# Optimization experiments

Measured on AMD Instinct MI355X. Metric: run time of the kernel, lower is better.

## Reference

```python
import jax, jax.numpy as jnp
import numpy as np

KQ = 512
NEG = -1e9


def setup_inputs() -> dict:
    key = jax.random.key(0)
    k1, k2, k3, k4, k5 = jax.random.split(key, 5)
    B, NQ, NK, D, V, O = 16, 1024, 2048, 512, 512, 256
    return {
        "keys": jax.random.normal(k1, (B, NK, D), dtype=jnp.float32),
        "queries": jax.random.normal(k2, (B, NQ, D), dtype=jnp.float32),
        "values": jax.random.normal(k3, (B, NK, V), dtype=jnp.float32),
        "mask": jax.random.randint(k4, (B, NQ, NK), 0, 2, dtype=jnp.int32),
        "W_resize": jax.random.normal(k5, (O, V), dtype=jnp.float32) * (1.0 / np.sqrt(V)),
        "b_resize": jnp.zeros((O,), dtype=jnp.float32),
    }


def reference(keys, queries, values, mask, W_resize, b_resize):
    # score: scaled dot product  [B, NQ, NK]
    logits = jnp.einsum("bqd,bkd->bqk", queries, keys) / jnp.sqrt(jnp.float32(KQ))
    logits = jnp.where(mask == 0, jnp.float32(NEG), logits)
    attn = jax.nn.softmax(logits, axis=-1)
    # context: [B, NQ, V]
    context = jnp.einsum("bqk,bkv->bqv", attn, values)
    # resize to out_size
    context = jnp.einsum("bqv,ov->bqo", context, W_resize) + b_resize
    return context
```

## Files before the change

### kernel.cpp

```cpp
#include <hip/hip_runtime.h>

#define BB   16
#define NQ   1024
#define NK   2048
#define DD   512
#define VV   512
#define OO   256
#define SCALE 0.044194173824159216f

typedef __attribute__((ext_vector_type(4))) float f32x4;
typedef __attribute__((ext_vector_type(8))) short s16x8;

#define AS1(p) ((const __attribute__((address_space(1))) void*)(p))
#define AS3(p) ((__attribute__((address_space(3))) void*)(p))

__device__ __forceinline__ unsigned short f2bf(float f) {
  unsigned u = __float_as_uint(f);
  u += 0x7fffu + ((u >> 16) & 1u);
  return (unsigned short)(u >> 16);
}
__device__ __forceinline__ float bf2f(unsigned short b) {
  return __uint_as_float(((unsigned)b) << 16);
}

__device__ __forceinline__ void gemm_bt_core(
    const unsigned short* __restrict__ Abase,
    const unsigned short* __restrict__ Bbase,
    int K,
    unsigned short* As, unsigned short* Bs,
    f32x4 acc[4][4])
{
  const int t = threadIdx.x;
  const int w = t >> 6;
  const int l = t & 63;
  const int srow = l >> 2;
  const int scol = (l & 3) * 8;
  const int r0 = (w * 2 + 0) * 16 + srow;
  const int r1 = (w * 2 + 1) * 16 + srow;
  const int lds0 = (w * 2 + 0) * 512 + l * 8;
  const int lds1 = (w * 2 + 1) * 512 + l * 8;
  const int wm = (w >> 1) * 64;
  const int wn = (w & 1) * 64;
  const int lm = l & 15;
  const int lq = l >> 4;

  for (int kt = 0; kt < K; kt += 32) {
    __builtin_amdgcn_global_load_lds(AS1(Abase + (size_t)r0 * K + kt + scol), AS3(As + lds0), 16, 0, 0);
    __builtin_amdgcn_global_load_lds(AS1(Abase + (size_t)r1 * K + kt + scol), AS3(As + lds1), 16, 0, 0);
    __builtin_amdgcn_global_load_lds(AS1(Bbase + (size_t)r0 * K + kt + scol), AS3(Bs + lds0), 16, 0, 0);
    __builtin_amdgcn_global_load_lds(AS1(Bbase + (size_t)r1 * K + kt + scol), AS3(Bs + lds1), 16, 0, 0);
    __syncthreads();
    s16x8 af[4], bfr[4];
    #pragma unroll
    for (int i = 0; i < 4; ++i) {
      af[i]  = *(const s16x8*)(As + (wm + i * 16 + lm) * 32 + lq * 8);
      bfr[i] = *(const s16x8*)(Bs + (wn + i * 16 + lm) * 32 + lq * 8);
    }
    #pragma unroll
    for (int mi = 0; mi < 4; ++mi)
      #pragma unroll
      for (int ni = 0; ni < 4; ++ni)
        acc[mi][ni] = __builtin_amdgcn_mfma_f32_16x16x32_bf16(af[mi], bfr[ni], acc[mi][ni], 0, 0, 0);
    __syncthreads();
  }
}


#define CS_STRIDE 136

__global__ __launch_bounds__(256)
void qk_kernel(const unsigned short* __restrict__ Qb,
               const unsigned short* __restrict__ Kb,
               const int* __restrict__ mask,
               unsigned short* __restrict__ S,
               float* __restrict__ sums)
{
  const int b  = blockIdx.z;
  const int tm = blockIdx.y;
  const int tn = blockIdx.x;
  __shared__ unsigned short smem[128 * CS_STRIDE];
  unsigned short* As = smem;
  unsigned short* Bs = smem + 4096;
  unsigned short* Cs = smem;
  f32x4 acc[4][4];
  #pragma unroll
  for (int i = 0; i < 4; ++i)
    #pragma unroll
    for (int j = 0; j < 4; ++j) acc[i][j] = (f32x4){0.f, 0.f, 0.f, 0.f};

  gemm_bt_core(Qb + ((size_t)b * NQ + tm * 128) * DD,
               Kb + ((size_t)b * NK + tn * 128) * DD, DD, As, Bs, acc);

  const int t = threadIdx.x, w = t >> 6, l = t & 63;
  const int wm = (w >> 1) * 64, wn = (w & 1) * 64;
  const int lm = l & 15, lq = l >> 4;
  #pragma unroll
  for (int mi = 0; mi < 4; ++mi)
    #pragma unroll
    for (int ni = 0; ni < 4; ++ni)
      #pragma unroll
      for (int r = 0; r < 4; ++r)
        Cs[(wm + mi * 16 + lq * 4 + r) * CS_STRIDE + wn + ni * 16 + lm] =
            f2bf(acc[mi][ni][r] * SCALE);
  __syncthreads();

  const int trow = t >> 4, tcol = (t & 15) * 8;
  #pragma unroll
  for (int it = 0; it < 8; ++it) {
    const int row = it * 16 + trow;
    const int gq = tm * 128 + row;
    const size_t gbase = ((size_t)b * NQ + gq) * NK + tn * 128 + tcol;
    s16x8 v = *(const s16x8*)(Cs + row * CS_STRIDE + tcol);
    const int4 m0 = *(const int4*)(mask + gbase);
    const int4 m1 = *(const int4*)(mask + gbase + 4);
    float e[8];
    e[0] = m0.x ? __expf(bf2f((unsigned short)v[0])) : 0.f;
    e[1] = m0.y ? __expf(bf2f((unsigned short)v[1])) : 0.f;
    e[2] = m0.z ? __expf(bf2f((unsigned short)v[2])) : 0.f;
    e[3] = m0.w ? __expf(bf2f((unsigned short)v[3])) : 0.f;
    e[4] = m1.x ? __expf(bf2f((unsigned short)v[4])) : 0.f;
    e[5] = m1.y ? __expf(bf2f((unsigned short)v[5])) : 0.f;
    e[6] = m1.z ? __expf(bf2f((unsigned short)v[6])) : 0.f;
    e[7] = m1.w ? __expf(bf2f((unsigned short)v[7])) : 0.f;
    float sp = 0.f;
    #pragma unroll
    for (int j = 0; j < 8; ++j) sp += e[j];
    #pragma unroll
    for (int off = 8; off > 0; off >>= 1) sp += __shfl_down(sp, off, 16);
    if ((t & 15) == 0) atomicAdd(&sums[(size_t)b * NQ + gq], sp);
    s16x8 o;
    #pragma unroll
    for (int j = 0; j < 8; ++j) o[j] = (short)f2bf(e[j]);
    *(s16x8*)(S + gbase) = o;
  }
}

__global__ __launch_bounds__(256)
void pv_kernel(const unsigned short* __restrict__ P,
               const unsigned short* __restrict__ Vt,
               const float* __restrict__ sums,
               unsigned short* __restrict__ Ctx)
{
  const int b  = blockIdx.z;
  const int tm = blockIdx.y;
  const int tn = blockIdx.x;
  __shared__ unsigned short smem[128 * CS_STRIDE];
  __shared__ float Ls[128];
  unsigned short* As = smem;
  unsigned short* Bs = smem + 4096;
  unsigned short* Cs = smem;
  const int t = threadIdx.x;
  if (t < 128) Ls[t] = 1.0f / sums[(size_t)b * NQ + tm * 128 + t];
  f32x4 acc[4][4];
  #pragma unroll
  for (int i = 0; i < 4; ++i)
    #pragma unroll
    for (int j = 0; j < 4; ++j) acc[i][j] = (f32x4){0.f, 0.f, 0.f, 0.f};

  gemm_bt_core(P  + ((size_t)b * NQ + tm * 128) * NK,
               Vt + ((size_t)b * VV + tn * 128) * NK, NK, As, Bs, acc);

  const int w = t >> 6, l = t & 63;
  const int wm = (w >> 1) * 64, wn = (w & 1) * 64;
  const int lm = l & 15, lq = l >> 4;
  #pragma unroll
  for (int mi = 0; mi < 4; ++mi)
    #pragma unroll
    for (int ni = 0; ni < 4; ++ni)
      #pragma unroll
      for (int r = 0; r < 4; ++r) {
        const int row = wm + mi * 16 + lq * 4 + r;
        Cs[row * CS_STRIDE + wn + ni * 16 + lm] = f2bf(acc[mi][ni][r] * Ls[row]);
      }
  __syncthreads();
  const int trow = t >> 4, tcol = (t & 15) * 8;
  #pragma unroll
  for (int it = 0; it < 8; ++it) {
    const int row = it * 16 + trow;
    s16x8 v = *(const s16x8*)(Cs + row * CS_STRIDE + tcol);
    *(s16x8*)(Ctx + ((size_t)b * NQ + tm * 128 + row) * VV + tn * 128 + tcol) = v;
  }
}

#define CSF_STRIDE 136
__global__ __launch_bounds__(256)
void rs_kernel(const unsigned short* __restrict__ Ctx,
               const unsigned short* __restrict__ Wb,
               const float* __restrict__ bias,
               float* __restrict__ out)
{
  const int tm = blockIdx.y;
  const int tn = blockIdx.x;
  __shared__ float smemf[128 * CSF_STRIDE];
  unsigned short* As = (unsigned short*)smemf;
  unsigned short* Bs = (unsigned short*)smemf + 4096;
  float* Cs = smemf;
  f32x4 acc[4][4];
  #pragma unroll
  for (int i = 0; i < 4; ++i)
    #pragma unroll
    for (int j = 0; j < 4; ++j) acc[i][j] = (f32x4){0.f, 0.f, 0.f, 0.f};

  gemm_bt_core(Ctx + (size_t)tm * 128 * VV,
               Wb + (size_t)tn * 128 * VV, VV, As, Bs, acc);

  const int t = threadIdx.x, w = t >> 6, l = t & 63;
  const int wm = (w >> 1) * 64, wn = (w & 1) * 64;
  const int lm = l & 15, lq = l >> 4;
  #pragma unroll
  for (int mi = 0; mi < 4; ++mi)
    #pragma unroll
    for (int ni = 0; ni < 4; ++ni)
      #pragma unroll
      for (int r = 0; r < 4; ++r)
        Cs[(wm + mi * 16 + lq * 4 + r) * CSF_STRIDE + wn + ni * 16 + lm] = acc[mi][ni][r];
  __syncthreads();
  const int trow = t >> 4, tcol = (t & 15) * 8;
  #pragma unroll
  for (int it = 0; it < 8; ++it) {
    const int row = it * 16 + trow;
    f32x4 a = *(const f32x4*)(Cs + row * CSF_STRIDE + tcol);
    f32x4 c = *(const f32x4*)(Cs + row * CSF_STRIDE + tcol + 4);
    const int gn = tn * 128 + tcol;
    const f32x4 b0 = *(const f32x4*)(bias + gn);
    const f32x4 b1 = *(const f32x4*)(bias + gn + 4);
    a += b0; c += b1;
    float* o = out + (size_t)(tm * 128 + row) * OO + gn;
    *(f32x4*)o = a;
    *(f32x4*)(o + 4) = c;
  }
}

__global__ __launch_bounds__(256)
void cvt_kernel(const float* __restrict__ in, unsigned short* __restrict__ out, int n8)
{
  const int i = blockIdx.x * 256 + threadIdx.x;
  if (i >= n8) return;
  const float4* p = (const float4*)in + (size_t)i * 2;
  const float4 a = p[0], b = p[1];
  s16x8 o;
  o[0] = (short)f2bf(a.x); o[1] = (short)f2bf(a.y);
  o[2] = (short)f2bf(a.z); o[3] = (short)f2bf(a.w);
  o[4] = (short)f2bf(b.x); o[5] = (short)f2bf(b.y);
  o[6] = (short)f2bf(b.z); o[7] = (short)f2bf(b.w);
  ((s16x8*)out)[i] = o;
}

#define VT_STRIDE 68
__global__ __launch_bounds__(256)
void vt_kernel(const float* __restrict__ V, unsigned short* __restrict__ Vt)
{
  const int b  = blockIdx.z;
  const int k0 = blockIdx.y * 64;
  const int v0 = blockIdx.x * 64;
  __shared__ float tile[64 * VT_STRIDE];
  const int t = threadIdx.x;
  const int lr = t >> 4, lc4 = (t & 15) * 4;
  #pragma unroll
  for (int j = 0; j < 4; ++j) {
    const int row = lr + j * 16;
    const float4 x = *(const float4*)(V + ((size_t)b * NK + k0 + row) * VV + v0 + lc4);
    *(float4*)(tile + row * VT_STRIDE + lc4) = x;
  }
  __syncthreads();
  const int vr = t >> 3, kx = (t & 7) * 8;
  #pragma unroll
  for (int j = 0; j < 2; ++j) {
    const int v = vr + j * 32;
    s16x8 o;
    #pragma unroll
    for (int i = 0; i < 8; ++i) o[i] = (short)f2bf(tile[(kx + i) * VT_STRIDE + v]);
    *(s16x8*)(Vt + ((size_t)b * VV + v0 + v) * NK + k0 + kx) = o;
  }
}

__global__ __launch_bounds__(256)
void zero_kernel(float* __restrict__ p, int n)
{
  const int i = blockIdx.x * 256 + threadIdx.x;
  if (i < n) p[i] = 0.f;
}

extern "C" void kernel_launch(void* const* d_in, const int* in_sizes, int n_in,
                              void* d_out, int out_size, void* d_ws, size_t ws_size,
                              hipStream_t stream)
{
  const float* keys    = (const float*)d_in[0];
  const float* queries = (const float*)d_in[1];
  const float* values  = (const float*)d_in[2];
  const int*   mask    = (const int*)  d_in[3];
  const float* W       = (const float*)d_in[4];
  const float* bias    = (const float*)d_in[5];
  float* out = (float*)d_out;

  char* ws = (char*)d_ws;
  unsigned short* Qb = (unsigned short*)(ws);
  unsigned short* Kb = (unsigned short*)(ws + (16ull << 20));
  unsigned short* Vt = (unsigned short*)(ws + (48ull << 20));
  unsigned short* Wb = (unsigned short*)(ws + (80ull << 20));
  unsigned short* S  = (unsigned short*)(ws + (81ull << 20));
  float* sums        = (float*)(ws + (145ull << 20));
  unsigned short* Ctx = Qb;

  cvt_kernel<<<dim3(4096), 256, 0, stream>>>(queries, Qb, (BB * NQ * DD) / 8);
  cvt_kernel<<<dim3(8192), 256, 0, stream>>>(keys, Kb, (BB * NK * DD) / 8);
  cvt_kernel<<<dim3(64),   256, 0, stream>>>(W, Wb, (OO * VV) / 8);
  vt_kernel<<<dim3(VV / 64, NK / 64, BB), 256, 0, stream>>>(values, Vt);
  zero_kernel<<<dim3(64), 256, 0, stream>>>(sums, BB * NQ);

  qk_kernel<<<dim3(NK / 128, NQ / 128, BB), 256, 0, stream>>>(Qb, Kb, mask, S, sums);
  pv_kernel<<<dim3(VV / 128, NQ / 128, BB), 256, 0, stream>>>(S, Vt, sums, Ctx);
  rs_kernel<<<dim3(OO / 128, (BB * NQ) / 128, 1), 256, 0, stream>>>(Ctx, Wb, bias, out);
}
```

Measured before the change: 460.9 us.

## Reassociate attention output projection as P·(V·Wᵀ) and merge kernel launches

Precomputes V·Wᵀ per batch (NK×256), so the attention-probability GEMM contracts against a 256-wide matrix instead of 512 and the separate resize GEMM disappears. The VW GEMM runs inside the same launch as the QK/softmax blocks, and all conversions plus the zeroing of sums are merged into one prep kernel. The V transpose is dropped because VWt is written already transposed. The cost is an extra bf16 rounding of V·W before the P product, a different accumulation order, and smaller 64-row tiles in the final GEMM.

```diff
diff --git a/kernel.cpp b/kernel.cpp
--- a/kernel.cpp
+++ b/kernel.cpp
@@ -22,6 +22,8 @@
 __device__ __forceinline__ float bf2f(unsigned short b) {
   return __uint_as_float(((unsigned)b) << 16);
 }
+
+#define MFMA16(a, b, c) __builtin_amdgcn_mfma_f32_16x16x32_bf16(a, b, c, 0, 0, 0)
 
 __device__ __forceinline__ void gemm_bt_core(
     const unsigned short* __restrict__ Abase,
@@ -60,7 +62,7 @@
     for (int mi = 0; mi < 4; ++mi)
       #pragma unroll
       for (int ni = 0; ni < 4; ++ni)
-        acc[mi][ni] = __builtin_amdgcn_mfma_f32_16x16x32_bf16(af[mi], bfr[ni], acc[mi][ni], 0, 0, 0);
+        acc[mi][ni] = MFMA16(af[mi], bfr[ni], acc[mi][ni]);
     __syncthreads();
   }
 }
@@ -69,173 +71,190 @@
 #define CS_STRIDE 136
 
 __global__ __launch_bounds__(256)
-void qk_kernel(const unsigned short* __restrict__ Qb,
-               const unsigned short* __restrict__ Kb,
-               const int* __restrict__ mask,
-               unsigned short* __restrict__ S,
-               float* __restrict__ sums)
-{
-  const int b  = blockIdx.z;
-  const int tm = blockIdx.y;
-  const int tn = blockIdx.x;
+void qkvw_kernel(const unsigned short* __restrict__ Qb,
+                 const unsigned short* __restrict__ Kb,
+                 const unsigned short* __restrict__ Vb,
+                 const unsigned short* __restrict__ Wb,
+                 const int* __restrict__ mask,
+                 unsigned short* __restrict__ P,
+                 unsigned short* __restrict__ VWt,
+                 float* __restrict__ sums)
+{
   __shared__ unsigned short smem[128 * CS_STRIDE];
   unsigned short* As = smem;
   unsigned short* Bs = smem + 4096;
   unsigned short* Cs = smem;
+  const int bid = blockIdx.x;
+  const int t = threadIdx.x, w = t >> 6, l = t & 63;
+  const int wm = (w >> 1) * 64, wn = (w & 1) * 64;
+  const int lm = l & 15, lq = l >> 4;
+  const int trow = t >> 4, tcol = (t & 15) * 8;
+
   f32x4 acc[4][4];
   #pragma unroll
   for (int i = 0; i < 4; ++i)
     #pragma unroll
     for (int j = 0; j < 4; ++j) acc[i][j] = (f32x4){0.f, 0.f, 0.f, 0.f};
 
-  gemm_bt_core(Qb + ((size_t)b * NQ + tm * 128) * DD,
-               Kb + ((size_t)b * NK + tn * 128) * DD, DD, As, Bs, acc);
+  if (bid < 2048) {
+    const int b  = bid >> 7;
+    const int tm = (bid >> 4) & 7;
+    const int tn = bid & 15;
+
+    gemm_bt_core(Qb + ((size_t)b * NQ + tm * 128) * DD,
+                 Kb + ((size_t)b * NK + tn * 128) * DD, DD, As, Bs, acc);
+
+    #pragma unroll
+    for (int mi = 0; mi < 4; ++mi)
+      #pragma unroll
+      for (int ni = 0; ni < 4; ++ni)
+        #pragma unroll
+        for (int r = 0; r < 4; ++r)
+          Cs[(wm + mi * 16 + lq * 4 + r) * CS_STRIDE + wn + ni * 16 + lm] =
+              f2bf(acc[mi][ni][r] * SCALE);
+    __syncthreads();
+
+    #pragma unroll
+    for (int it = 0; it < 8; ++it) {
+      const int row = it * 16 + trow;
+      const int gq = tm * 128 + row;
+      const size_t gbase = ((size_t)b * NQ + gq) * NK + tn * 128 + tcol;
+      s16x8 v = *(const s16x8*)(Cs + row * CS_STRIDE + tcol);
+      const int4 m0 = *(const int4*)(mask + gbase);
+      const int4 m1 = *(const int4*)(mask + gbase + 4);
+      float e[8];
+      e[0] = m0.x ? __expf(bf2f((unsigned short)v[0])) : 0.f;
+      e[1] = m0.y ? __expf(bf2f((unsigned short)v[1])) : 0.f;
+      e[2] = m0.z ? __expf(bf2f((unsigned short)v[2])) : 0.f;
+      e[3] = m0.w ? __expf(bf2f((unsigned short)v[3])) : 0.f;
+      e[4] = m1.x ? __expf(bf2f((unsigned short)v[4])) : 0.f;
+      e[5] = m1.y ? __expf(bf2f((unsigned short)v[5])) : 0.f;
+      e[6] = m1.z ? __expf(bf2f((unsigned short)v[6])) : 0.f;
+      e[7] = m1.w ? __expf(bf2f((unsigned short)v[7])) : 0.f;
+      float sp = 0.f;
+      #pragma unroll
+      for (int j = 0; j < 8; ++j) sp += e[j];
+      #pragma unroll
+      for (int off = 8; off > 0; off >>= 1) sp += __shfl_down(sp, off, 16);
+      if ((t & 15) == 0) atomicAdd(&sums[(size_t)b * NQ + gq], sp);
+      s16x8 o;
+      #pragma unroll
+      for (int j = 0; j < 8; ++j) o[j] = (short)f2bf(e[j]);
+      *(s16x8*)(P + gbase) = o;
+    }
+  } else {
+    const int vid = bid - 2048;
+    const int b  = vid >> 5;
+    const int kt = (vid >> 1) & 15;
+    const int ot = vid & 1;
+
+    gemm_bt_core(Vb + ((size_t)b * NK + kt * 128) * VV,
+                 Wb + (size_t)ot * 128 * VV, VV, As, Bs, acc);
+
+    #pragma unroll
+    for (int mi = 0; mi < 4; ++mi)
+      #pragma unroll
+      for (int ni = 0; ni < 4; ++ni)
+        #pragma unroll
+        for (int r = 0; r < 4; ++r)
+          Cs[(wn + ni * 16 + lm) * CS_STRIDE + wm + mi * 16 + lq * 4 + r] =
+              f2bf(acc[mi][ni][r]);
+    __syncthreads();
+
+    #pragma unroll
+    for (int it = 0; it < 8; ++it) {
+      const int orow = it * 16 + trow;
+      s16x8 v = *(const s16x8*)(Cs + orow * CS_STRIDE + tcol);
+      *(s16x8*)(VWt + ((size_t)b * OO + ot * 128 + orow) * NK + kt * 128 + tcol) = v;
+    }
+  }
+}
+
+#define PW_STRIDE 132
+__global__ __launch_bounds__(256)
+void pvw_kernel(const unsigned short* __restrict__ P,
+                const unsigned short* __restrict__ VWt,
+                const float* __restrict__ sums,
+                const float* __restrict__ bias,
+                float* __restrict__ out)
+{
+  const int ot = blockIdx.x;
+  const int qt = blockIdx.y;
+  const int b  = blockIdx.z;
+  __shared__ float Csf[64 * PW_STRIDE];
+  __shared__ float Ls[64];
+  unsigned short* As = (unsigned short*)Csf;
+  unsigned short* Bs = (unsigned short*)Csf + 2048;
 
   const int t = threadIdx.x, w = t >> 6, l = t & 63;
-  const int wm = (w >> 1) * 64, wn = (w & 1) * 64;
+  const int wr = w >> 1, wc = w & 1;
   const int lm = l & 15, lq = l >> 4;
+  if (t < 64) Ls[t] = 1.0f / sums[(size_t)b * NQ + qt * 64 + t];
+
+  f32x4 acc[2][4];
   #pragma unroll
-  for (int mi = 0; mi < 4; ++mi)
+  for (int i = 0; i < 2; ++i)
+    #pragma unroll
+    for (int j = 0; j < 4; ++j) acc[i][j] = (f32x4){0.f, 0.f, 0.f, 0.f};
+
+  const unsigned short* Abase = P   + ((size_t)b * NQ + qt * 64) * NK;
+  const unsigned short* Bbase = VWt + ((size_t)b * OO + ot * 128) * NK;
+  const int ar = t >> 2, ac = (t & 3) * 8;
+  const int br0 = (w * 2 + 0) * 16 + (l >> 2);
+  const int br1 = (w * 2 + 1) * 16 + (l >> 2);
+  const int bc = (l & 3) * 8;
+  const int bld0 = (w * 2 + 0) * 512 + l * 8;
+  const int bld1 = (w * 2 + 1) * 512 + l * 8;
+
+  for (int k0 = 0; k0 < NK; k0 += 32) {
+    __builtin_amdgcn_global_load_lds(AS1(Abase + (size_t)ar * NK + k0 + ac), AS3(As + t * 8), 16, 0, 0);
+    __builtin_amdgcn_global_load_lds(AS1(Bbase + (size_t)br0 * NK + k0 + bc), AS3(Bs + bld0), 16, 0, 0);
+    __builtin_amdgcn_global_load_lds(AS1(Bbase + (size_t)br1 * NK + k0 + bc), AS3(Bs + bld1), 16, 0, 0);
+    __syncthreads();
+    s16x8 af[2], bfr[4];
+    #pragma unroll
+    for (int mi = 0; mi < 2; ++mi)
+      af[mi] = *(const s16x8*)(As + (wr * 32 + mi * 16 + lm) * 32 + lq * 8);
     #pragma unroll
     for (int ni = 0; ni < 4; ++ni)
-      #pragma unroll
-      for (int r = 0; r < 4; ++r)
-        Cs[(wm + mi * 16 + lq * 4 + r) * CS_STRIDE + wn + ni * 16 + lm] =
-            f2bf(acc[mi][ni][r] * SCALE);
-  __syncthreads();
-
-  const int trow = t >> 4, tcol = (t & 15) * 8;
+      bfr[ni] = *(const s16x8*)(Bs + (wc * 64 + ni * 16 + lm) * 32 + lq * 8);
+    #pragma unroll
+    for (int mi = 0; mi < 2; ++mi)
+      #pragma unroll
+      for (int ni = 0; ni < 4; ++ni)
+        acc[mi][ni] = MFMA16(af[mi], bfr[ni], acc[mi][ni]);
+    __syncthreads();
+  }
+
   #pragma unroll
-  for (int it = 0; it < 8; ++it) {
-    const int row = it * 16 + trow;
-    const int gq = tm * 128 + row;
-    const size_t gbase = ((size_t)b * NQ + gq) * NK + tn * 128 + tcol;
-    s16x8 v = *(const s16x8*)(Cs + row * CS_STRIDE + tcol);
-    const int4 m0 = *(const int4*)(mask + gbase);
-    const int4 m1 = *(const int4*)(mask + gbase + 4);
-    float e[8];
-    e[0] = m0.x ? __expf(bf2f((unsigned short)v[0])) : 0.f;
-    e[1] = m0.y ? __expf(bf2f((unsigned short)v[1])) : 0.f;
-    e[2] = m0.z ? __expf(bf2f((unsigned short)v[2])) : 0.f;
-    e[3] = m0.w ? __expf(bf2f((unsigned short)v[3])) : 0.f;
-    e[4] = m1.x ? __expf(bf2f((unsigned short)v[4])) : 0.f;
-    e[5] = m1.y ? __expf(bf2f((unsigned short)v[5])) : 0.f;
-    e[6] = m1.z ? __expf(bf2f((unsigned short)v[6])) : 0.f;
-    e[7] = m1.w ? __expf(bf2f((unsigned short)v[7])) : 0.f;
-    float sp = 0.f;
-    #pragma unroll
-    for (int j = 0; j < 8; ++j) sp += e[j];
-    #pragma unroll
-    for (int off = 8; off > 0; off >>= 1) sp += __shfl_down(sp, off, 16);
-    if ((t & 15) == 0) atomicAdd(&sums[(size_t)b * NQ + gq], sp);
-    s16x8 o;
-    #pragma unroll
-    for (int j = 0; j < 8; ++j) o[j] = (short)f2bf(e[j]);
-    *(s16x8*)(S + gbase) = o;
-  }
-}
-
-__global__ __launch_bounds__(256)
-void pv_kernel(const unsigned short* __restrict__ P,
-               const unsigned short* __restrict__ Vt,
-               const float* __restrict__ sums,
-               unsigned short* __restrict__ Ctx)
-{
-  const int b  = blockIdx.z;
-  const int tm = blockIdx.y;
-  const int tn = blockIdx.x;
-  __shared__ unsigned short smem[128 * CS_STRIDE];
-  __shared__ float Ls[128];
-  unsigned short* As = smem;
-  unsigned short* Bs = smem + 4096;
-  unsigned short* Cs = smem;
-  const int t = threadIdx.x;
-  if (t < 128) Ls[t] = 1.0f / sums[(size_t)b * NQ + tm * 128 + t];
-  f32x4 acc[4][4];
-  #pragma unroll
-  for (int i = 0; i < 4; ++i)
-    #pragma unroll
-    for (int j = 0; j < 4; ++j) acc[i][j] = (f32x4){0.f, 0.f, 0.f, 0.f};
-
-  gemm_bt_core(P  + ((size_t)b * NQ + tm * 128) * NK,
-               Vt + ((size_t)b * VV + tn * 128) * NK, NK, As, Bs, acc);
-
-  const int w = t >> 6, l = t & 63;
-  const int wm = (w >> 1) * 64, wn = (w & 1) * 64;
-  const int lm = l & 15, lq = l >> 4;
-  #pragma unroll
-  for (int mi = 0; mi < 4; ++mi)
+  for (int mi = 0; mi < 2; ++mi)
     #pragma unroll
     for (int ni = 0; ni < 4; ++ni)
       #pragma unroll
       for (int r = 0; r < 4; ++r) {
-        const int row = wm + mi * 16 + lq * 4 + r;
-        Cs[row * CS_STRIDE + wn + ni * 16 + lm] = f2bf(acc[mi][ni][r] * Ls[row]);
+        const int row = wr * 32 + mi * 16 + lq * 4 + r;
+        const int col = wc * 64 + ni * 16 + lm;
+        Csf[row * PW_STRIDE + col] = acc[mi][ni][r] * Ls[row];
       }
   __syncthreads();
-  const int trow = t >> 4, tcol = (t & 15) * 8;
+  const int trow = t >> 2;
   #pragma unroll
-  for (int it = 0; it < 8; ++it) {
-    const int row = it * 16 + trow;
-    s16x8 v = *(const s16x8*)(Cs + row * CS_STRIDE + tcol);
-    *(s16x8*)(Ctx + ((size_t)b * NQ + tm * 128 + row) * VV + tn * 128 + tcol) = v;
-  }
-}
-
-#define CSF_STRIDE 136
-__global__ __launch_bounds__(256)
-void rs_kernel(const unsigned short* __restrict__ Ctx,
-               const unsigned short* __restrict__ Wb,
-               const float* __restrict__ bias,
-               float* __restrict__ out)
-{
-  const int tm = blockIdx.y;
-  const int tn = blockIdx.x;
-  __shared__ float smemf[128 * CSF_STRIDE];
-  unsigned short* As = (unsigned short*)smemf;
-  unsigned short* Bs = (unsigned short*)smemf + 4096;
-  float* Cs = smemf;
-  f32x4 acc[4][4];
-  #pragma unroll
-  for (int i = 0; i < 4; ++i)
-    #pragma unroll
-    for (int j = 0; j < 4; ++j) acc[i][j] = (f32x4){0.f, 0.f, 0.f, 0.f};
-
-  gemm_bt_core(Ctx + (size_t)tm * 128 * VV,
-               Wb + (size_t)tn * 128 * VV, VV, As, Bs, acc);
-
-  const int t = threadIdx.x, w = t >> 6, l = t & 63;
-  const int wm = (w >> 1) * 64, wn = (w & 1) * 64;
-  const int lm = l & 15, lq = l >> 4;
-  #pragma unroll
-  for (int mi = 0; mi < 4; ++mi)
-    #pragma unroll
-    for (int ni = 0; ni < 4; ++ni)
-      #pragma unroll
-      for (int r = 0; r < 4; ++r)
-        Cs[(wm + mi * 16 + lq * 4 + r) * CSF_STRIDE + wn + ni * 16 + lm] = acc[mi][ni][r];
-  __syncthreads();
-  const int trow = t >> 4, tcol = (t & 15) * 8;
-  #pragma unroll
-  for (int it = 0; it < 8; ++it) {
-    const int row = it * 16 + trow;
-    f32x4 a = *(const f32x4*)(Cs + row * CSF_STRIDE + tcol);
-    f32x4 c = *(const f32x4*)(Cs + row * CSF_STRIDE + tcol + 4);
-    const int gn = tn * 128 + tcol;
-    const f32x4 b0 = *(const f32x4*)(bias + gn);
-    const f32x4 b1 = *(const f32x4*)(bias + gn + 4);
-    a += b0; c += b1;
-    float* o = out + (size_t)(tm * 128 + row) * OO + gn;
+  for (int it = 0; it < 4; ++it) {
+    const int col = (t & 3) * 8 + it * 32;
+    f32x4 a = *(const f32x4*)(Csf + trow * PW_STRIDE + col);
+    f32x4 c = *(const f32x4*)(Csf + trow * PW_STRIDE + col + 4);
+    const int go = ot * 128 + col;
+    a += *(const f32x4*)(bias + go);
+    c += *(const f32x4*)(bias + go + 4);
+    float* o = out + ((size_t)b * NQ + qt * 64 + trow) * OO + go;
     *(f32x4*)o = a;
     *(f32x4*)(o + 4) = c;
   }
 }
 
-__global__ __launch_bounds__(256)
-void cvt_kernel(const float* __restrict__ in, unsigned short* __restrict__ out, int n8)
-{
-  const int i = blockIdx.x * 256 + threadIdx.x;
-  if (i >= n8) return;
+__device__ __forceinline__ void cvt8(const float* __restrict__ in,
+                                     unsigned short* __restrict__ out, int i)
+{
   const float4* p = (const float4*)in + (size_t)i * 2;
   const float4 a = p[0], b = p[1];
   s16x8 o;
@@ -246,39 +265,27 @@
   ((s16x8*)out)[i] = o;
 }
 
-#define VT_STRIDE 68
 __global__ __launch_bounds__(256)
-void vt_kernel(const float* __restrict__ V, unsigned short* __restrict__ Vt)
-{
-  const int b  = blockIdx.z;
-  const int k0 = blockIdx.y * 64;
-  const int v0 = blockIdx.x * 64;
-  __shared__ float tile[64 * VT_STRIDE];
+void prep_kernel(const float* __restrict__ q, const float* __restrict__ k,
+                 const float* __restrict__ v, const float* __restrict__ w,
+                 unsigned short* __restrict__ Qb, unsigned short* __restrict__ Kb,
+                 unsigned short* __restrict__ Vb, unsigned short* __restrict__ Wb,
+                 float* __restrict__ sums)
+{
+  const int bid = blockIdx.x;
   const int t = threadIdx.x;
-  const int lr = t >> 4, lc4 = (t & 15) * 4;
-  #pragma unroll
-  for (int j = 0; j < 4; ++j) {
-    const int row = lr + j * 16;
-    const float4 x = *(const float4*)(V + ((size_t)b * NK + k0 + row) * VV + v0 + lc4);
-    *(float4*)(tile + row * VT_STRIDE + lc4) = x;
-  }
-  __syncthreads();
-  const int vr = t >> 3, kx = (t & 7) * 8;
-  #pragma unroll
-  for (int j = 0; j < 2; ++j) {
-    const int v = vr + j * 32;
-    s16x8 o;
-    #pragma unroll
-    for (int i = 0; i < 8; ++i) o[i] = (short)f2bf(tile[(kx + i) * VT_STRIDE + v]);
-    *(s16x8*)(Vt + ((size_t)b * VV + v0 + v) * NK + k0 + kx) = o;
-  }
-}
-
-__global__ __launch_bounds__(256)
-void zero_kernel(float* __restrict__ p, int n)
-{
-  const int i = blockIdx.x * 256 + threadIdx.x;
-  if (i < n) p[i] = 0.f;
+  if (bid < 4096) {
+    cvt8(q, Qb, bid * 256 + t);
+  } else if (bid < 12288) {
+    cvt8(k, Kb, (bid - 4096) * 256 + t);
+  } else if (bid < 20480) {
+    cvt8(v, Vb, (bid - 12288) * 256 + t);
+  } else if (bid < 20544) {
+    cvt8(w, Wb, (bid - 20480) * 256 + t);
+  } else {
+    const int i = (bid - 20544) * 256 + t;
+    if (i < BB * NQ) sums[i] = 0.f;
+  }
 }
 
 extern "C" void kernel_launch(void* const* d_in, const int* in_sizes, int n_in,
@@ -294,21 +301,16 @@
   float* out = (float*)d_out;
 
   char* ws = (char*)d_ws;
-  unsigned short* Qb = (unsigned short*)(ws);
-  unsigned short* Kb = (unsigned short*)(ws + (16ull << 20));
-  unsigned short* Vt = (unsigned short*)(ws + (48ull << 20));
-  unsigned short* Wb = (unsigned short*)(ws + (80ull << 20));
-  unsigned short* S  = (unsigned short*)(ws + (81ull << 20));
-  float* sums        = (float*)(ws + (145ull << 20));
-  unsigned short* Ctx = Qb;
-
-  cvt_kernel<<<dim3(4096), 256, 0, stream>>>(queries, Qb, (BB * NQ * DD) / 8);
-  cvt_kernel<<<dim3(8192), 256, 0, stream>>>(keys, Kb, (BB * NK * DD) / 8);
-  cvt_kernel<<<dim3(64),   256, 0, stream>>>(W, Wb, (OO * VV) / 8);
-  vt_kernel<<<dim3(VV / 64, NK / 64, BB), 256, 0, stream>>>(values, Vt);
-  zero_kernel<<<dim3(64), 256, 0, stream>>>(sums, BB * NQ);
-
-  qk_kernel<<<dim3(NK / 128, NQ / 128, BB), 256, 0, stream>>>(Qb, Kb, mask, S, sums);
-  pv_kernel<<<dim3(VV / 128, NQ / 128, BB), 256, 0, stream>>>(S, Vt, sums, Ctx);
-  rs_kernel<<<dim3(OO / 128, (BB * NQ) / 128, 1), 256, 0, stream>>>(Ctx, Wb, bias, out);
-}
+  unsigned short* Qb  = (unsigned short*)(ws);
+  unsigned short* Kb  = (unsigned short*)(ws + (16ull << 20));
+  unsigned short* Vb  = (unsigned short*)(ws + (48ull << 20));
+  unsigned short* Wb  = (unsigned short*)(ws + (80ull << 20));
+  unsigned short* VWt = (unsigned short*)(ws + (81ull << 20));
+  unsigned short* P   = (unsigned short*)(ws + (97ull << 20));
+  float* sums         = (float*)(ws + (161ull << 20));
+
+  prep_kernel<<<dim3(20608), 256, 0, stream>>>(queries, keys, values, W,
+                                               Qb, Kb, Vb, Wb, sums);
+  qkvw_kernel<<<dim3(2560), 256, 0, stream>>>(Qb, Kb, Vb, Wb, mask, P, VWt, sums);
+  pvw_kernel<<<dim3(OO / 128, NQ / 64, BB), 256, 0, stream>>>(P, VWt, sums, bias, out);
+}
```

Result: faster. 424.1 us (-8.0%).
